# Optimization experiments

Measured on AMD Instinct MI355X. Metric: run time of the kernel, lower is better.

Reference implementation:

```python
import jax, jax.numpy as jnp
import numpy as np

NUM_HEADS = 16
HEAD_DIM = 64  # hidden_size // num_heads


def _logsparse_allowed(seq_len):
    # allowed[i, j] True if key j is attended by query i:
    # j == i, j == i-1, or j == i - 2^k (k >= 1); combined with causal (j <= i).
    i = jnp.arange(seq_len)[:, None]
    j = jnp.arange(seq_len)[None, :]
    diff = i - j
    pow2 = (diff > 0) & ((diff & (diff - 1)) == 0)  # covers diff==1 and diff==2^k
    return (diff == 0) | pow2  # implies diff >= 0, so causal is subsumed


def setup_inputs() -> dict:
    key = jax.random.key(0)
    ks = jax.random.split(key, 7)
    B, S, H = 4, 2048, 1024
    return {
        "hidden_states": jax.random.normal(ks[0], (B, S, H), dtype=jnp.float32),
        "attention_mask": jnp.zeros((B, 1, 1, S), dtype=jnp.float32),
        "Wq": jax.random.normal(ks[1], (H, H), dtype=jnp.float32) * 0.02,
        "bq": jnp.zeros((H,), dtype=jnp.float32),
        "Wk": jax.random.normal(ks[2], (H, H), dtype=jnp.float32) * 0.02,
        "bk": jnp.zeros((H,), dtype=jnp.float32),
        "Wv": jax.random.normal(ks[3], (H, H), dtype=jnp.float32) * 0.02,
        "bv": jnp.zeros((H,), dtype=jnp.float32),
    }


def _split_heads(x):
    B, S, _ = x.shape
    return x.reshape(B, S, NUM_HEADS, HEAD_DIM).transpose(0, 2, 1, 3)  # b h t d


def reference(hidden_states, attention_mask, Wq, bq, Wk, bk, Wv, bv):
    B, S, H = hidden_states.shape
    q = _split_heads(hidden_states @ Wq.T + bq)
    k = _split_heads(hidden_states @ Wk.T + bk)
    v = _split_heads(hidden_states @ Wv.T + bv)

    scores = jnp.einsum("bhqd,bhkd->bhqk", q, k) * (HEAD_DIM ** -0.5)
    allowed = _logsparse_allowed(S)  # [S, S] bool
    scores = jnp.where(allowed[None, None], scores, -jnp.inf)
    scores = scores + attention_mask  # [B,1,1,S] additive mask
    probs = jax.nn.softmax(scores, axis=-1)
    out = jnp.einsum("bhqk,bhkd->bhqd", probs, v)
    return out.transpose(0, 2, 1, 3).reshape(B, S, H)
```

## Files before the change

### kernel.cpp

```cpp
#include <hip/hip_runtime.h>
#include <hip/hip_bf16.h>

#define S_LEN   2048
#define NHEADS  16
#define HDIM    64
#define HID     1024
#define BATCH   4
#define M_ROWS  (BATCH * S_LEN)

typedef __attribute__((ext_vector_type(8))) short short8;
typedef __attribute__((ext_vector_type(4))) float floatx4;
typedef __attribute__((ext_vector_type(4))) unsigned short ushort4v;

__device__ __forceinline__ unsigned short f2bf_rne(float x) {
  union { float f; unsigned u; } v; v.f = x;
  unsigned r = v.u + 0x7fffu + ((v.u >> 16) & 1u);
  return (unsigned short)(r >> 16);
}

__device__ __forceinline__ float bf2f(unsigned short u) {
  union { unsigned u; float f; } c; c.u = ((unsigned)u) << 16;
  return c.f;
}

__device__ __forceinline__ void glds16(const unsigned short* g, unsigned short* l) {
  __builtin_amdgcn_global_load_lds(
      (const __attribute__((address_space(1))) unsigned int*)g,
      (__attribute__((address_space(3))) unsigned int*)l, 16, 0, 0);
}

#define HS4 (M_ROWS * HID / 4)
#define W4  (HID * HID / 4)
__global__ __launch_bounds__(256) void cast_all(
    const float* __restrict__ hs, const float* __restrict__ Wq,
    const float* __restrict__ Wk, const float* __restrict__ Wv,
    unsigned short* __restrict__ hsb, unsigned short* __restrict__ wqb,
    unsigned short* __restrict__ wkb, unsigned short* __restrict__ wvb) {
  int idx = blockIdx.x * 256 + threadIdx.x;
  const float* in;
  unsigned short* out;
  int off;
  if (idx < HS4) {
    in = hs; out = hsb; off = idx;
  } else {
    int r = idx - HS4;
    int seg = r >> 18;
    off = r & (W4 - 1);
    in  = (seg == 0) ? Wq  : (seg == 1) ? Wk  : Wv;
    out = (seg == 0) ? wqb : (seg == 1) ? wkb : wvb;
  }
  floatx4 v = __builtin_nontemporal_load((const floatx4*)in + off);
  ushort4v o;
  o.x = f2bf_rne(v.x);
  o.y = f2bf_rne(v.y);
  o.z = f2bf_rne(v.z);
  o.w = f2bf_rne(v.w);
  ((ushort4v*)out)[off] = o;
}

__global__ __launch_bounds__(256, 2) void qkv_gemm(
    const unsigned short* __restrict__ A,
    const unsigned short* __restrict__ W0, const unsigned short* __restrict__ W1,
    const unsigned short* __restrict__ W2,
    const float* __restrict__ b0, const float* __restrict__ b1,
    const float* __restrict__ b2,
    unsigned short* __restrict__ O0, unsigned short* __restrict__ O1,
    unsigned short* __restrict__ O2) {
  const int K = HID;
  const int N = HID;

  __shared__ __align__(16) unsigned short lds[3 * 12288];

  const int tid = threadIdx.x;
  const int w = tid >> 6;
  const int lane = tid & 63;

  const int bid = blockIdx.x;
  const int xcd = bid & 7;
  const int rr  = bid >> 3;
  const int sb  = rr >> 5;
  const int q   = rr & 31;
  const int sbid = xcd * 3 + sb;
  const int mg = sbid & 7;
  const int sg = sbid >> 3;
  const int mi   = mg * 4 + (q & 3);
  const int slab = sg * 8 + (q >> 2);
  const int ni = slab & 7;
  const int z  = slab >> 3;
  const int m0 = mi << 8;
  const int n0 = ni << 7;

  const unsigned short* __restrict__ Wz = (z == 0) ? W0 : (z == 1) ? W1 : W2;
  const float* __restrict__ bias = (z == 0) ? b0 : (z == 1) ? b1 : b2;
  unsigned short* __restrict__ O = (z == 0) ? O0 : (z == 1) ? O1 : O2;

  const int lr = lane >> 2;
  const int gc = (lane & 3) ^ ((lr >> 1) & 3);
  const unsigned short* gsrc[6];
  unsigned short* ldst[6];
  #pragma unroll
  for (int u = 0; u < 6; ++u) {
    const int seg = w * 6 + u;
    if (seg < 16) {
      gsrc[u] = A + (size_t)(m0 + seg * 16 + lr) * K + gc * 8;
    } else {
      gsrc[u] = Wz + (size_t)(n0 + (seg - 16) * 16 + lr) * K + gc * 8;
    }
    ldst[u] = lds + seg * 512;
  }

  auto stage = [&](int t) {
    const int bofs = (t % 3) * 12288;
    const int ko = t * 32;
    #pragma unroll
    for (int u = 0; u < 6; ++u)
      glds16(gsrc[u] + ko, ldst[u] + bofs);
  };

  const int lrow = lane & 15;
  const int qd = lane >> 4;
  const int cp = (qd ^ ((lrow >> 1) & 3)) * 8;
  const int wm = w & 1;
  const int wn = w >> 1;
  const int arow = wm * 128 + lrow;
  const int brow = wn * 64 + lrow;

  floatx4 acc[8][4] = {};

  stage(0);
  stage(1);

  for (int t = 0; t < 32; ++t) {
    asm volatile("s_waitcnt lgkmcnt(0)" ::: "memory");
    if (t < 31) asm volatile("s_waitcnt vmcnt(6)" ::: "memory");
    else        asm volatile("s_waitcnt vmcnt(0)" ::: "memory");
    __builtin_amdgcn_s_barrier();
    asm volatile("" ::: "memory");

    const unsigned short* Asb = lds + (t % 3) * 12288;
    const unsigned short* Bsb = Asb + 8192;

    if (t + 2 < 32) stage(t + 2);

    short8 af[8], bf[4];
    #pragma unroll
    for (int im = 0; im < 8; ++im)
      af[im] = *(const short8*)(Asb + (arow + im * 16) * 32 + cp);
    #pragma unroll
    for (int in = 0; in < 4; ++in)
      bf[in] = *(const short8*)(Bsb + (brow + in * 16) * 32 + cp);

    __builtin_amdgcn_s_setprio(1);
    #pragma unroll
    for (int im = 0; im < 8; ++im)
      #pragma unroll
      for (int in = 0; in < 4; ++in)
        acc[im][in] = __builtin_amdgcn_mfma_f32_16x16x32_bf16(af[im], bf[in], acc[im][in], 0, 0, 0);
    __builtin_amdgcn_s_setprio(0);
  }

  #pragma unroll
  for (int im = 0; im < 8; ++im) {
    #pragma unroll
    for (int in = 0; in < 4; ++in) {
      const int col = n0 + wn * 64 + in * 16 + lrow;
      const float bb = bias[col];
      #pragma unroll
      for (int r = 0; r < 4; ++r) {
        const int row = m0 + wm * 128 + im * 16 + (qd << 2) + r;
        O[(size_t)row * N + col] = f2bf_rne(acc[im][in][r] + bb);
      }
    }
  }
}

__global__ __launch_bounds__(256) void logsparse_attn(
    const unsigned short* __restrict__ Q, const unsigned short* __restrict__ K,
    const unsigned short* __restrict__ V, const float* __restrict__ mask,
    float* __restrict__ out) {
  const int bid = (blockIdx.x & 7) * 512 + (blockIdx.x >> 3);
  const int tid = threadIdx.x;
  const int l = tid & 7;
  const int qglob = bid * 32 + (tid >> 3);

  const int i = qglob & (S_LEN - 1);
  const int h = (qglob >> 11) & (NHEADS - 1);
  const int b = qglob >> 15;

  const size_t base = (size_t)b * S_LEN * HID + h * HDIM + l * 8;

  int js[12];
  js[0] = i;
  int nj = 1;
  for (int d = 1; d <= i; d <<= 1) js[nj++] = i - d;
  #pragma unroll
  for (int t = 0; t < 12; ++t)
    if (t >= nj) js[t] = i;

  short8 k8[12];
  #pragma unroll
  for (int t = 0; t < 12; ++t)
    k8[t] = *(const short8*)(K + base + (size_t)js[t] * HID);
  const short8 q8 = *(const short8*)(Q + base + (size_t)i * HID);
  float mk[12];
  #pragma unroll
  for (int t = 0; t < 12; ++t)
    mk[t] = mask[b * S_LEN + js[t]];

  float qf[8];
  #pragma unroll
  for (int e = 0; e < 8; ++e) qf[e] = bf2f((unsigned short)q8[e]);

  float s[12];
  #pragma unroll
  for (int t = 0; t < 12; ++t) {
    float p = 0.f;
    #pragma unroll
    for (int e = 0; e < 8; ++e) p += qf[e] * bf2f((unsigned short)k8[t][e]);
    p += __shfl_xor(p, 1, 64);
    p += __shfl_xor(p, 2, 64);
    p += __shfl_xor(p, 4, 64);
    s[t] = (t < nj) ? (p * 0.125f + mk[t]) : -1e30f;
  }

  float mx = s[0];
  #pragma unroll
  for (int t = 1; t < 12; ++t) mx = fmaxf(mx, s[t]);
  float lsum = 0.f;
  #pragma unroll
  for (int t = 0; t < 12; ++t) { s[t] = __expf(s[t] - mx); lsum += s[t]; }
  const float inv = 1.f / lsum;

  short8 v8[12];
  #pragma unroll
  for (int t = 0; t < 12; ++t)
    v8[t] = *(const short8*)(V + base + (size_t)js[t] * HID);

  float o[8] = {};
  #pragma unroll
  for (int t = 0; t < 12; ++t) {
    #pragma unroll
    for (int e = 0; e < 8; ++e) o[e] += s[t] * bf2f((unsigned short)v8[t][e]);
  }

  float* op = out + base + (size_t)i * HID;
  floatx4 o0 = {o[0] * inv, o[1] * inv, o[2] * inv, o[3] * inv};
  floatx4 o1 = {o[4] * inv, o[5] * inv, o[6] * inv, o[7] * inv};
  __builtin_nontemporal_store(o0, (floatx4*)op);
  __builtin_nontemporal_store(o1, (floatx4*)(op + 4));
}

extern "C" void kernel_launch(void* const* d_in, const int* in_sizes, int n_in,
                              void* d_out, int out_size, void* d_ws, size_t ws_size,
                              hipStream_t stream) {
  const float* hs   = (const float*)d_in[0];
  const float* mask = (const float*)d_in[1];
  const float* Wq   = (const float*)d_in[2];
  const float* bq   = (const float*)d_in[3];
  const float* Wk   = (const float*)d_in[4];
  const float* bk   = (const float*)d_in[5];
  const float* Wv   = (const float*)d_in[6];
  const float* bv   = (const float*)d_in[7];
  float* out = (float*)d_out;

  unsigned short* hsb = (unsigned short*)d_ws;
  unsigned short* wqb = hsb + (size_t)M_ROWS * HID;
  unsigned short* wkb = wqb + (size_t)HID * HID;
  unsigned short* wvb = wkb + (size_t)HID * HID;
  unsigned short* Qb = wvb + (size_t)HID * HID;
  unsigned short* Kb = Qb + (size_t)M_ROWS * HID;
  unsigned short* Vb = Kb + (size_t)M_ROWS * HID;

  {
    int quads = HS4 + 3 * W4;
    cast_all<<<quads / 256, 256, 0, stream>>>(hs, Wq, Wk, Wv, hsb, wqb, wkb, wvb);
  }

  {
    qkv_gemm<<<768, 256, 0, stream>>>(hsb, wqb, wkb, wvb, bq, bk, bv, Qb, Kb, Vb);
  }

  {
    int blocks = (BATCH * NHEADS * S_LEN) / 32;
    logsparse_attn<<<blocks, 256, 0, stream>>>(Qb, Kb, Vb, mask, out);
  }
}
```

Baseline: 180.2 us.

## Use 8 waves per GEMM block with a 4-stage LDS pipeline

The QKV GEMM block grows from 256 to 512 threads. Each wave now owns a 64x64 output tile instead of 128x64, and the LDS ring buffer grows from 3 to 4 stages with a prefetch distance of 3. The main loop drops the lgkmcnt wait and handles the tail with explicit vmcnt drains. The aim is to hide global-load latency better and raise wave-level parallelism, at the cost of more LDS per block and possibly lower occupancy (about 96KB LDS per block).

```diff
diff --git a/kernel.cpp b/kernel.cpp
--- a/kernel.cpp
+++ b/kernel.cpp
@@ -58,7 +58,7 @@
   ((ushort4v*)out)[off] = o;
 }
 
-__global__ __launch_bounds__(256, 2) void qkv_gemm(
+__global__ __launch_bounds__(512, 2) void qkv_gemm(
     const unsigned short* __restrict__ A,
     const unsigned short* __restrict__ W0, const unsigned short* __restrict__ W1,
     const unsigned short* __restrict__ W2,
@@ -69,7 +69,7 @@
   const int K = HID;
   const int N = HID;
 
-  __shared__ __align__(16) unsigned short lds[3 * 12288];
+  __shared__ __align__(16) unsigned short lds[4 * 12288];
 
   const int tid = threadIdx.x;
   const int w = tid >> 6;
@@ -96,11 +96,11 @@
 
   const int lr = lane >> 2;
   const int gc = (lane & 3) ^ ((lr >> 1) & 3);
-  const unsigned short* gsrc[6];
-  unsigned short* ldst[6];
-  #pragma unroll
-  for (int u = 0; u < 6; ++u) {
-    const int seg = w * 6 + u;
+  const unsigned short* gsrc[3];
+  unsigned short* ldst[3];
+  #pragma unroll
+  for (int u = 0; u < 3; ++u) {
+    const int seg = w * 3 + u;
     if (seg < 16) {
       gsrc[u] = A + (size_t)(m0 + seg * 16 + lr) * K + gc * 8;
     } else {
@@ -109,65 +109,73 @@
     ldst[u] = lds + seg * 512;
   }
 
-  auto stage = [&](int t) {
-    const int bofs = (t % 3) * 12288;
-    const int ko = t * 32;
-    #pragma unroll
-    for (int u = 0; u < 6; ++u)
+  auto stage = [&](int h) {
+    const int bofs = (h & 3) * 12288;
+    const int ko = h * 32;
+    #pragma unroll
+    for (int u = 0; u < 3; ++u)
       glds16(gsrc[u] + ko, ldst[u] + bofs);
   };
 
   const int lrow = lane & 15;
   const int qd = lane >> 4;
   const int cp = (qd ^ ((lrow >> 1) & 3)) * 8;
-  const int wm = w & 1;
-  const int wn = w >> 1;
-  const int arow = wm * 128 + lrow;
-  const int brow = wn * 64 + lrow;
-
-  floatx4 acc[8][4] = {};
-
-  stage(0);
-  stage(1);
-
-  for (int t = 0; t < 32; ++t) {
-    asm volatile("s_waitcnt lgkmcnt(0)" ::: "memory");
-    if (t < 31) asm volatile("s_waitcnt vmcnt(6)" ::: "memory");
-    else        asm volatile("s_waitcnt vmcnt(0)" ::: "memory");
-    __builtin_amdgcn_s_barrier();
-    asm volatile("" ::: "memory");
-
-    const unsigned short* Asb = lds + (t % 3) * 12288;
+  const int arow = (w & 3) * 64 + lrow;
+  const int brow = (w >> 2) * 64 + lrow;
+
+  floatx4 acc[4][4] = {};
+
+  auto half_body = [&](int h, bool pf) {
+    const unsigned short* Asb = lds + (h & 3) * 12288;
     const unsigned short* Bsb = Asb + 8192;
-
-    if (t + 2 < 32) stage(t + 2);
-
-    short8 af[8], bf[4];
-    #pragma unroll
-    for (int im = 0; im < 8; ++im)
+    if (pf) stage(h + 3);
+    short8 af[4], bf[4];
+    #pragma unroll
+    for (int im = 0; im < 4; ++im)
       af[im] = *(const short8*)(Asb + (arow + im * 16) * 32 + cp);
     #pragma unroll
     for (int in = 0; in < 4; ++in)
       bf[in] = *(const short8*)(Bsb + (brow + in * 16) * 32 + cp);
-
     __builtin_amdgcn_s_setprio(1);
     #pragma unroll
-    for (int im = 0; im < 8; ++im)
+    for (int im = 0; im < 4; ++im)
       #pragma unroll
       for (int in = 0; in < 4; ++in)
         acc[im][in] = __builtin_amdgcn_mfma_f32_16x16x32_bf16(af[im], bf[in], acc[im][in], 0, 0, 0);
     __builtin_amdgcn_s_setprio(0);
-  }
-
-  #pragma unroll
-  for (int im = 0; im < 8; ++im) {
+  };
+
+  stage(0); stage(1); stage(2);
+
+  #pragma unroll 4
+  for (int h = 0; h < 29; ++h) {
+    asm volatile("s_waitcnt vmcnt(6)" ::: "memory");
+    __builtin_amdgcn_s_barrier();
+    asm volatile("" ::: "memory");
+    half_body(h, true);
+  }
+  asm volatile("s_waitcnt vmcnt(6)" ::: "memory");
+  __builtin_amdgcn_s_barrier();
+  asm volatile("" ::: "memory");
+  half_body(29, false);
+  asm volatile("s_waitcnt vmcnt(3)" ::: "memory");
+  __builtin_amdgcn_s_barrier();
+  asm volatile("" ::: "memory");
+  half_body(30, false);
+  asm volatile("s_waitcnt vmcnt(0)" ::: "memory");
+  __builtin_amdgcn_s_barrier();
+  asm volatile("" ::: "memory");
+  half_body(31, false);
+
+  #pragma unroll
+  for (int im = 0; im < 4; ++im) {
     #pragma unroll
     for (int in = 0; in < 4; ++in) {
-      const int col = n0 + wn * 64 + in * 16 + lrow;
+      const int col = n0 + (w >> 2) * 64 + in * 16 + lrow;
       const float bb = bias[col];
       #pragma unroll
       for (int r = 0; r < 4; ++r) {
-        const int row = m0 + wm * 128 + im * 16 + (qd << 2) + r;
+        const int row = m0 + (w & 3) * 64 + im * 16 + (qd << 2) + r;
         O[(size_t)row * N + col] = f2bf_rne(acc[im][in][r] + bb);
       }
     }
@@ -277,7 +285,7 @@
   }
 
   {
-    qkv_gemm<<<768, 256, 0, stream>>>(hsb, wqb, wkb, wvb, bq, bk, bv, Qb, Kb, Vb);
+    qkv_gemm<<<768, 512, 0, stream>>>(hsb, wqb, wkb, wvb, bq, bk, bv, Qb, Kb, Vb);
   }
 
   {
```

Result: slower. 185.3 us (+2.8%).
